# Performance work log

Hardware: AMD Instinct MI355X
Metric: run time of the kernel (lower is better)

Reference implementation:

```python
import jax, jax.numpy as jnp
import numpy as np

GROUPS = 32
HEADS = 8
EPS = 1e-5


def group_norm(x, w, b):
    B, C, H, W = x.shape
    xg = x.reshape(B, GROUPS, C // GROUPS, H, W)
    mu = xg.mean(axis=(2, 3, 4), keepdims=True)
    var = xg.var(axis=(2, 3, 4), keepdims=True)
    xn = ((xg - mu) * jax.lax.rsqrt(var + EPS)).reshape(B, C, H, W)
    return xn * w[None, :, None, None] + b[None, :, None, None]


def conv1x1(x, w, b):
    # w: [out_c, in_c], x: [B, C, H, W]
    return jnp.einsum('oc,bchw->bohw', w, x) + b[None, :, None, None]


def setup_inputs() -> dict:
    key = jax.random.key(0)
    ks = jax.random.split(key, 10)
    B, C, H, W = 8, 512, 32, 32
    s = 1.0 / np.sqrt(C)
    inp = {
        'x': jax.random.normal(ks[0], (B, C, H, W), dtype=jnp.float32),
        'gn_w': jnp.ones((C,), jnp.float32),
        'gn_b': jnp.zeros((C,), jnp.float32),
        'qw': jax.random.uniform(ks[1], (C, C), jnp.float32, -s, s),
        'qb': jax.random.uniform(ks[2], (C,), jnp.float32, -s, s),
        'kw': jax.random.uniform(ks[3], (C, C), jnp.float32, -s, s),
        'kb': jax.random.uniform(ks[4], (C,), jnp.float32, -s, s),
        'vw': jax.random.uniform(ks[5], (C, C), jnp.float32, -s, s),
        'vb': jax.random.uniform(ks[6], (C,), jnp.float32, -s, s),
        'ow': jax.random.uniform(ks[7], (C, C), jnp.float32, -s, s),
        'ob': jax.random.uniform(ks[8], (C,), jnp.float32, -s, s),
    }
    return inp


def reference(x, gn_w, gn_b, qw, qb, kw, kb, vw, vb, ow, ob):
    B, C, H, W = x.shape
    hd = C // HEADS          # head_dim
    N = H * W                # spatial tokens
    scale = float(hd) ** -0.5

    xn = group_norm(x, gn_w, gn_b)
    q = conv1x1(xn, qw, qb).reshape(B, HEADS, hd, N)
    k = conv1x1(xn, kw, kb).reshape(B, HEADS, hd, N)
    v = conv1x1(xn, vw, vb).reshape(B, HEADS, hd, N)

    # scores[b,h,n,m] = scale * <q[:, :, :, n], k[:, :, :, m]>
    scores = jnp.einsum('bhdn,bhdm->bhnm', q * scale, k)
    attn = jax.nn.softmax(scores, axis=-1)
    # out[b,h,d,n] = sum_m attn[b,h,n,m] * v[b,h,d,m]
    out = jnp.einsum('bhnm,bhdm->bhdn', attn, v).reshape(B, C, H, W)
    out = conv1x1(out, ow, ob)
    return out + x
```

## Files before the change

### kernel.cpp

```cpp
#include <hip/hip_runtime.h>
#include <cstdint>


typedef unsigned short u16;
typedef __attribute__((ext_vector_type(8)))  __bf16 bf16x8;
typedef __attribute__((ext_vector_type(4)))  float  f32x4;
typedef __attribute__((ext_vector_type(16))) float  f32x16;

typedef __attribute__((address_space(1))) const unsigned int guint;
typedef __attribute__((address_space(3))) unsigned int       luint;

__device__ __forceinline__ u16 f2bf(float f) {
  union { float f; unsigned u; } a; a.f = f;
  unsigned r = a.u + 0x7fffu + ((a.u >> 16) & 1u);
  return (u16)(r >> 16);
}

__device__ __forceinline__ unsigned pkbf(float a, float b) {
  unsigned short lo = __builtin_bit_cast(unsigned short, (__bf16)a);
  unsigned short hi = __builtin_bit_cast(unsigned short, (__bf16)b);
  return (unsigned)lo | ((unsigned)hi << 16);
}

__device__ __forceinline__ void plswap(unsigned &a, unsigned &b) {
  asm("v_permlane32_swap_b32 %0, %1" : "+v"(a), "+v"(b));
}

__device__ __forceinline__ void gload16(u16* lds_dst, const u16* g_src) {
  __builtin_amdgcn_global_load_lds((guint*)g_src, (luint*)lds_dst, 16, 0, 0);
}

__global__ __launch_bounds__(256) void gn_stats(const float* __restrict__ x,
                                                float* __restrict__ pstat) {
  int id = blockIdx.x;
  int bg = id >> 1, chunk = id & 1;
  int tid = threadIdx.x;
  const float* xg = x + ((size_t)(bg * 16 + chunk * 8)) * 1024;
  float s1 = 0.f, s2 = 0.f;
#pragma unroll
  for (int it = 0; it < 8; ++it) {
    f32x4 v = *(const f32x4*)(xg + it * 1024 + tid * 4);
    s1 += (v[0] + v[1]) + (v[2] + v[3]);
    s2 += (v[0] * v[0] + v[1] * v[1]) + (v[2] * v[2] + v[3] * v[3]);
  }
#pragma unroll
  for (int d = 32; d; d >>= 1) { s1 += __shfl_down(s1, d, 64); s2 += __shfl_down(s2, d, 64); }
  __shared__ float redw[4][2];
  if ((tid & 63) == 0) { redw[tid >> 6][0] = s1; redw[tid >> 6][1] = s2; }
  __syncthreads();
  if (tid == 0) {
    float t1 = redw[0][0] + redw[1][0] + redw[2][0] + redw[3][0];
    float t2 = redw[0][1] + redw[1][1] + redw[2][1] + redw[3][1];
    pstat[(bg * 2 + chunk) * 2 + 0] = t1;
    pstat[(bg * 2 + chunk) * 2 + 1] = t2;
  }
}

__global__ __launch_bounds__(256) void gn_apply(const float* __restrict__ x,
                                                const float* __restrict__ pstat,
                                                const float* __restrict__ gw,
                                                const float* __restrict__ gb,
                                                u16* __restrict__ xnT) {
  __shared__ u16 tr[64 * 130];
  int id = blockIdx.x;
  int cs = id & 3, ntl = (id >> 2) & 15, b = id >> 6;
  int tid = threadIdx.x;
  int tc = tid >> 1, th = tid & 1;
  int c = cs * 128 + tc, g = c >> 4;
  float a1 = pstat[(b * 32 + g) * 4 + 0], a2 = pstat[(b * 32 + g) * 4 + 1];
  float b1 = pstat[(b * 32 + g) * 4 + 2], b2 = pstat[(b * 32 + g) * 4 + 3];
  float s1 = a1 + b1, s2 = a2 + b2;
  float mean = s1 * (1.f / 16384.f);
  float var  = s2 * (1.f / 16384.f) - mean * mean;
  float rinv = rsqrtf(var + 1e-5f);
  float wgt = gw[c] * rinv;
  float bia = gb[c] - mean * wgt;
  const float* src = x + ((size_t)(b * 512 + c)) * 1024 + ntl * 64 + th * 32;
#pragma unroll
  for (int i = 0; i < 8; ++i) {
    f32x4 v = *(const f32x4*)(src + i * 4);
#pragma unroll
    for (int j = 0; j < 4; ++j)
      tr[(th * 32 + i * 4 + j) * 130 + tc] = f2bf(v[j] * wgt + bia);
  }
  __syncthreads();
  int n = tid >> 2, q = tid & 3;
  u16* dst = xnT + (size_t)b * 524288 + (size_t)(ntl * 64 + n) * 512 + cs * 128 + q * 32;
#pragma unroll
  for (int wd = 0; wd < 16; ++wd)
    *(unsigned*)&dst[wd * 2] = *(const unsigned*)&tr[n * 130 + q * 32 + wd * 2];
}

__global__ __launch_bounds__(256) void cvtw_kernel(const float* __restrict__ q,
                                                   const float* __restrict__ k,
                                                   const float* __restrict__ v,
                                                   const float* __restrict__ o,
                                                   u16* __restrict__ dst) {
  int i = blockIdx.x * 256 + threadIdx.x;
  int wsel = i >> 16;
  const float* src = wsel == 0 ? q : wsel == 1 ? k : wsel == 2 ? v : o;
  f32x4 val = *(const f32x4*)(src + (size_t)(i & 65535) * 4);
  u16 r0 = f2bf(val[0]), r1 = f2bf(val[1]), r2 = f2bf(val[2]), r3 = f2bf(val[3]);
  unsigned lo = (unsigned)r0 | ((unsigned)r1 << 16);
  unsigned hi = (unsigned)r2 | ((unsigned)r3 << 16);
  unsigned long long pk = (unsigned long long)lo | ((unsigned long long)hi << 32);
  *(unsigned long long*)(dst + (size_t)i * 4) = pk;
}

__global__ __launch_bounds__(256) void gemm_qkv(
    const u16* __restrict__ xnT, const u16* __restrict__ Wc,
    const float* __restrict__ qb, const float* __restrict__ kb,
    const float* __restrict__ vb,
    u16* __restrict__ Qs, u16* __restrict__ Ks, u16* __restrict__ Vs) {
  __shared__ u16 smem[32768];
  int id = blockIdx.x;
  int xcd = id & 7, slot = id >> 3;
  int g12 = slot / 12, q12 = slot % 12;
  int p = xcd * 8 + g12;
  int b = p & 7, yt = p >> 3;
  int xt = q12 & 3, which = q12 >> 2;

  const u16* Ab = xnT + (size_t)b * 524288 + (size_t)yt * 128 * 512;
  const u16* Bb = Wc + which * 262144 + (size_t)xt * 128 * 512;
  const float* bias = which == 0 ? qb : (which == 1 ? kb : vb);
  float scale = which == 0 ? 0.18033688011112043f : 1.0f;

  int tid = threadIdx.x, w = tid >> 6, lane = tid & 63;
  int wr = w >> 1, wcn = w & 1;
  int srow = lane >> 3, sk8 = (lane & 7) ^ srow;
  f32x4 acc[4][4] = {};

#define QKV_STAGE(buf, k0)                                                     \
  {                                                                            \
    u16* lA_ = smem + (buf) * 8192;                                            \
    u16* lB_ = smem + 16384 + (buf) * 8192;                                    \
    _Pragma("unroll")                                                          \
    for (int c2 = 0; c2 < 4; ++c2) {                                           \
      int ck = w * 4 + c2;                                                     \
      gload16(&lA_[ck * 512], Ab + (size_t)(ck * 8 + srow) * 512 + (k0) + sk8 * 8); \
      gload16(&lB_[ck * 512], Bb + (size_t)(ck * 8 + srow) * 512 + (k0) + sk8 * 8); \
    }                                                                          \
  }

  QKV_STAGE(0, 0);
  __syncthreads();
  for (int t = 0; t < 8; ++t) {
    if (t < 7) QKV_STAGE((t + 1) & 1, (t + 1) * 64);
    const u16* lA = smem + (t & 1) * 8192;
    const u16* lB = smem + 16384 + (t & 1) * 8192;
#pragma unroll
    for (int ks = 0; ks < 2; ++ks) {
      int k8 = ks * 4 + (lane >> 4);
      bf16x8 af[4], bfr[4];
#pragma unroll
      for (int mf = 0; mf < 4; ++mf) {
        int row = wr * 64 + mf * 16 + (lane & 15);
        af[mf] = *(const bf16x8*)&lA[row * 64 + ((k8 ^ (row & 7)) * 8)];
      }
#pragma unroll
      for (int nf = 0; nf < 4; ++nf) {
        int row = wcn * 64 + nf * 16 + (lane & 15);
        bfr[nf] = *(const bf16x8*)&lB[row * 64 + ((k8 ^ (row & 7)) * 8)];
      }
#pragma unroll
      for (int mf = 0; mf < 4; ++mf)
#pragma unroll
        for (int nf = 0; nf < 4; ++nf)
          acc[mf][nf] = __builtin_amdgcn_mfma_f32_16x16x32_bf16(af[mf], bfr[nf], acc[mf][nf], 0, 0, 0);
    }
    __syncthreads();
  }
#undef QKV_STAGE

  if (which < 2) {
    u16* dst = (which == 0 ? Qs : Ks) + (size_t)b * 524288;
#pragma unroll
    for (int mf = 0; mf < 4; ++mf)
#pragma unroll
      for (int nf = 0; nf < 4; ++nf) {
        int cc = xt * 128 + wcn * 64 + nf * 16 + (lane & 15);
        float bv = bias[cc];
#pragma unroll
        for (int j = 0; j < 4; ++j) {
          int rr = yt * 128 + wr * 64 + mf * 16 + (lane >> 4) * 4 + j;
          dst[(size_t)rr * 512 + cc] = f2bf((acc[mf][nf][j] + bv) * scale);
        }
      }
  } else {
    u16* tr = smem;
#pragma unroll
    for (int mf = 0; mf < 4; ++mf)
#pragma unroll
      for (int nf = 0; nf < 4; ++nf) {
        int cc_t = wcn * 64 + nf * 16 + (lane & 15);
        float bv = bias[xt * 128 + cc_t];
#pragma unroll
        for (int j = 0; j < 4; ++j) {
          int rr_t = wr * 64 + mf * 16 + (lane >> 4) * 4 + j;
          tr[cc_t * 136 + rr_t] = f2bf(acc[mf][nf][j] + bv);
        }
      }
    __syncthreads();
    int r = tid >> 1, half = tid & 1;
    size_t base = (size_t)b * 524288 + (size_t)(xt * 128 + r) * 1024 + yt * 128 + half * 64;
#pragma unroll
    for (int i = 0; i < 8; ++i) {
      bf16x8 v = *(const bf16x8*)&tr[r * 136 + half * 64 + i * 8];
      *(bf16x8*)&Vs[base + i * 8] = v;
    }
  }
}

__global__ __launch_bounds__(256) void attn_kernel(const u16* __restrict__ Q,
                                                   const u16* __restrict__ Kt,
                                                   const u16* __restrict__ V,
                                                   u16* __restrict__ AO) {
  __shared__ __align__(16) u16 lK[2][8192];
  __shared__ __align__(16) u16 lV[2][8192];
  int id = blockIdx.x;
  int xcd = id & 7, slot = id >> 3;
  int bh = xcd * 8 + (slot >> 3);
  int nt = slot & 7;
  int b = bh >> 3, h = bh & 7;
  int tid = threadIdx.x, w = tid >> 6, lane = tid & 63;
  int l31 = lane & 31, lh = lane >> 5, r7 = l31 & 7;
  int nb = nt * 128 + w * 32;
  const u16* Qb = Q  + (size_t)b * 524288;
  const u16* Kb = Kt + (size_t)b * 524288 + h * 64;
  const u16* Vb = V  + (size_t)b * 524288 + (size_t)(h * 64) * 1024;

  int srowK = lane >> 3, sblkK = (lane & 7) ^ srowK;
  int srowV = lane >> 4;

  int kblk[4];
#pragma unroll
  for (int kc = 0; kc < 4; ++kc) kblk[kc] = ((kc * 2 + lh) ^ r7) * 8;

  bf16x8 bq[4];
#pragma unroll
  for (int kc = 0; kc < 4; ++kc)
    bq[kc] = *(const bf16x8*)&Qb[(size_t)(nb + l31) * 512 + h * 64 + kc * 16 + lh * 8];

  union { unsigned u[4]; bf16x8 v; } uo;
  uo.u[0] = uo.u[1] = uo.u[2] = uo.u[3] = 0x3F803F80u;
  bf16x8 vones = uo.v;

  f32x16 o0 = {}, o1 = {}, osum = {};

#define ATTN_STAGE(buf, m0)                                                    \
  {                                                                            \
    _Pragma("unroll")                                                          \
    for (int c2 = 0; c2 < 4; ++c2) {                                           \
      int ck = w * 4 + c2;                                                     \
      gload16(&lK[buf][ck * 512],                                              \
              Kb + (size_t)((m0) + ck * 8 + srowK) * 512 + sblkK * 8);         \
      int rv = ck * 4 + srowV;                                                 \
      int bvb = (lane & 15) ^ (rv & 7);                                        \
      gload16(&lV[buf][ck * 512], Vb + (size_t)rv * 1024 + (m0) + bvb * 8);    \
    }                                                                          \
  }

  ATTN_STAGE(0, 0);
  __syncthreads();
  for (int mt = 0; mt < 8; ++mt) {
    int cur = mt & 1;
    if (mt < 7) ATTN_STAGE(cur ^ 1, (mt + 1) * 128);
    const u16* kb = lK[cur];
    const u16* vb = lV[cur];
#pragma unroll
    for (int mb = 0; mb < 4; ++mb) {
      f32x16 s = {};
      int krow = (mb * 32 + l31) * 64;
#pragma unroll
      for (int kc = 0; kc < 4; ++kc) {
        bf16x8 ak = *(const bf16x8*)&kb[krow + kblk[kc]];
        s = __builtin_amdgcn_mfma_f32_32x32x16_bf16(ak, bq[kc], s, 0, 0, 0);
      }
      float p[16];
#pragma unroll
      for (int i = 0; i < 16; ++i) p[i] = exp2f(s[i]);
      unsigned A0 = pkbf(p[0], p[1]),  B0 = pkbf(p[4], p[5]);
      unsigned A1 = pkbf(p[2], p[3]),  B1 = pkbf(p[6], p[7]);
      unsigned A2 = pkbf(p[8], p[9]),  B2 = pkbf(p[12], p[13]);
      unsigned A3 = pkbf(p[10], p[11]), B3 = pkbf(p[14], p[15]);
      plswap(A0, B0); plswap(A1, B1); plswap(A2, B2); plswap(A3, B3);
      union { unsigned u[4]; bf16x8 v; } f0, f1;
      f0.u[0] = A0; f0.u[1] = A1; f0.u[2] = B0; f0.u[3] = B1;
      f1.u[0] = A2; f1.u[1] = A3; f1.u[2] = B2; f1.u[3] = B3;
#pragma unroll
      for (int kc = 0; kc < 2; ++kc) {
        bf16x8 pa = kc ? f1.v : f0.v;
        int vb0 = ((mb * 4 + kc * 2 + lh) ^ r7) * 8;
        bf16x8 v0 = *(const bf16x8*)&vb[(l31) * 128 + vb0];
        bf16x8 v1 = *(const bf16x8*)&vb[(32 + l31) * 128 + vb0];
        o0 = __builtin_amdgcn_mfma_f32_32x32x16_bf16(pa, v0, o0, 0, 0, 0);
        o1 = __builtin_amdgcn_mfma_f32_32x32x16_bf16(pa, v1, o1, 0, 0, 0);
        osum = __builtin_amdgcn_mfma_f32_32x32x16_bf16(pa, vones, osum, 0, 0, 0);
      }
    }
    __syncthreads();
  }
#undef ATTN_STAGE

  size_t base = (size_t)b * 524288;
#pragma unroll
  for (int i = 0; i < 16; ++i) {
    float rl = 1.0f / osum[i];
    int n = nb + (i & 3) + 8 * (i >> 2) + 4 * lh;
    size_t rowb = base + (size_t)n * 512 + h * 64;
    AO[rowb + l31]      = f2bf(o0[i] * rl);
    AO[rowb + 32 + l31] = f2bf(o1[i] * rl);
  }
}

__global__ __launch_bounds__(256) void gemm_proj(
    const u16* __restrict__ Wo, const u16* __restrict__ AO,
    const float* __restrict__ ob, const float* __restrict__ x,
    float* __restrict__ out) {
  __shared__ u16 smem[24576];
  int id = blockIdx.x;
  int xcd = id & 7, slot = id >> 3;
  int g8 = slot >> 3, y = slot & 7;
  int p = xcd * 8 + g8;
  int b = p & 7, xt = p >> 3;

  const u16* Ab = Wo + (size_t)y * 64 * 512;
  const u16* Bb = AO + (size_t)b * 524288 + (size_t)xt * 128 * 512;

  int tid = threadIdx.x, w = tid >> 6, lane = tid & 63;
  int wr = w >> 1, wcn = w & 1;
  int srow = lane >> 3, sk8 = (lane & 7) ^ srow;
  f32x4 acc[2][4] = {};

#define PROJ_STAGE(buf, k0)                                                    \
  {                                                                            \
    u16* lA_ = smem + (buf) * 4096;                                            \
    u16* lB_ = smem + 8192 + (buf) * 8192;                                     \
    _Pragma("unroll")                                                          \
    for (int c2 = 0; c2 < 6; ++c2) {                                           \
      int ck = w * 6 + c2;                                                     \
      if (ck < 8)                                                              \
        gload16(&lA_[ck * 512], Ab + (size_t)(ck * 8 + srow) * 512 + (k0) + sk8 * 8); \
      else                                                                     \
        gload16(&lB_[(ck - 8) * 512], Bb + (size_t)((ck - 8) * 8 + srow) * 512 + (k0) + sk8 * 8); \
    }                                                                          \
  }

  PROJ_STAGE(0, 0);
  __syncthreads();
  for (int t = 0; t < 8; ++t) {
    if (t < 7) PROJ_STAGE((t + 1) & 1, (t + 1) * 64);
    const u16* lA = smem + (t & 1) * 4096;
    const u16* lB = smem + 8192 + (t & 1) * 8192;
#pragma unroll
    for (int ks = 0; ks < 2; ++ks) {
      int k8 = ks * 4 + (lane >> 4);
      bf16x8 af[2], bfr[4];
#pragma unroll
      for (int mf = 0; mf < 2; ++mf) {
        int row = wr * 32 + mf * 16 + (lane & 15);
        af[mf] = *(const bf16x8*)&lA[row * 64 + ((k8 ^ (row & 7)) * 8)];
      }
#pragma unroll
      for (int nf = 0; nf < 4; ++nf) {
        int row = wcn * 64 + nf * 16 + (lane & 15);
        bfr[nf] = *(const bf16x8*)&lB[row * 64 + ((k8 ^ (row & 7)) * 8)];
      }
#pragma unroll
      for (int mf = 0; mf < 2; ++mf)
#pragma unroll
        for (int nf = 0; nf < 4; ++nf)
          acc[mf][nf] = __builtin_amdgcn_mfma_f32_16x16x32_bf16(af[mf], bfr[nf], acc[mf][nf], 0, 0, 0);
    }
    __syncthreads();
  }
#undef PROJ_STAGE

#pragma unroll
  for (int mf = 0; mf < 2; ++mf)
#pragma unroll
    for (int nf = 0; nf < 4; ++nf) {
      int cc = xt * 128 + wcn * 64 + nf * 16 + (lane & 15);
#pragma unroll
      for (int j = 0; j < 4; ++j) {
        int rr = y * 64 + wr * 32 + mf * 16 + (lane >> 4) * 4 + j;
        size_t idx = (size_t)b * 524288 + (size_t)rr * 1024 + cc;
        out[idx] = acc[mf][nf][j] + ob[rr] + x[idx];
      }
    }
}

extern "C" void kernel_launch(void* const* d_in, const int* in_sizes, int n_in,
                              void* d_out, int out_size, void* d_ws, size_t ws_size,
                              hipStream_t stream) {
  const float* x   = (const float*)d_in[0];
  const float* gnw = (const float*)d_in[1];
  const float* gnb = (const float*)d_in[2];
  const float* qw  = (const float*)d_in[3];
  const float* qb  = (const float*)d_in[4];
  const float* kw  = (const float*)d_in[5];
  const float* kb  = (const float*)d_in[6];
  const float* vw  = (const float*)d_in[7];
  const float* vb  = (const float*)d_in[8];
  const float* ow  = (const float*)d_in[9];
  const float* ob  = (const float*)d_in[10];
  float* out = (float*)d_out;

  u16* ws  = (u16*)d_ws;
  u16* xnT = ws;
  u16* Qs  = ws + 4194304;
  u16* Ks  = ws + 8388608;
  u16* Vs  = ws + 12582912;
  u16* Wc  = ws + 16777216;
  float* pstat = (float*)(ws + 17825792);
  u16* AO  = xnT;

  gn_stats<<<512, 256, 0, stream>>>(x, pstat);
  gn_apply<<<512, 256, 0, stream>>>(x, pstat, gnw, gnb, xnT);
  cvtw_kernel<<<1024, 256, 0, stream>>>(qw, kw, vw, ow, Wc);
  gemm_qkv<<<768, 256, 0, stream>>>(xnT, Wc, qb, kb, vb, Qs, Ks, Vs);
  attn_kernel<<<512, 256, 0, stream>>>(Qs, Ks, Vs, AO);
  gemm_proj<<<512, 256, 0, stream>>>(Wc + 786432, AO, ob, x, out);
}
```

Measured before the change: 166.7 us.

## Replace ones-MFMA row sum with lane sums and shrink attention KV tiles

Drops the third MFMA per PV step, which multiplied P by a vector of ones to get softmax denominators. Each lane now sums its exp values in scalar registers, the two half-waves are combined with a shuffle, and the result is redistributed through a small per-wave LDS buffer. The KV tile shrinks from 128 to 64 keys, halving LDS use, with a padded, swizzled layout shared by K and V. s_setprio hints are placed around the MFMA blocks. This cuts matrix-core work and LDS footprint, at the cost of more loop iterations and barriers plus extra VALU adds.

```diff
diff --git a/kernel.cpp b/kernel.cpp
--- a/kernel.cpp
+++ b/kernel.cpp
@@ -215,8 +215,9 @@
                                                    const u16* __restrict__ Kt,
                                                    const u16* __restrict__ V,
                                                    u16* __restrict__ AO) {
-  __shared__ __align__(16) u16 lK[2][8192];
-  __shared__ __align__(16) u16 lV[2][8192];
+  __shared__ __align__(16) u16 lK[2][4160];
+  __shared__ __align__(16) u16 lV[2][4160];
+  __shared__ __align__(16) float lsum[4][32];
   int id = blockIdx.x;
   int xcd = id & 7, slot = id >> 3;
   int bh = xcd * 8 + (slot >> 3);
@@ -229,87 +230,97 @@
   const u16* Kb = Kt + (size_t)b * 524288 + h * 64;
   const u16* Vb = V  + (size_t)b * 524288 + (size_t)(h * 64) * 1024;
 
-  int srowK = lane >> 3, sblkK = (lane & 7) ^ srowK;
-  int srowV = lane >> 4;
-
-  int kblk[4];
-#pragma unroll
-  for (int kc = 0; kc < 4; ++kc) kblk[kc] = ((kc * 2 + lh) ^ r7) * 8;
-
+  int lrow = lane >> 3, lblk = (lane & 7) ^ lrow;
+
+  int kbase = (l31 >> 3) * 520 + r7 * 64;
   bf16x8 bq[4];
 #pragma unroll
   for (int kc = 0; kc < 4; ++kc)
     bq[kc] = *(const bf16x8*)&Qb[(size_t)(nb + l31) * 512 + h * 64 + kc * 16 + lh * 8];
 
-  union { unsigned u[4]; bf16x8 v; } uo;
-  uo.u[0] = uo.u[1] = uo.u[2] = uo.u[3] = 0x3F803F80u;
-  bf16x8 vones = uo.v;
-
-  f32x16 o0 = {}, o1 = {}, osum = {};
+  f32x16 o0 = {}, o1 = {};
+  float lpart = 0.f;
 
 #define ATTN_STAGE(buf, m0)                                                    \
   {                                                                            \
     _Pragma("unroll")                                                          \
-    for (int c2 = 0; c2 < 4; ++c2) {                                           \
-      int ck = w * 4 + c2;                                                     \
-      gload16(&lK[buf][ck * 512],                                              \
-              Kb + (size_t)((m0) + ck * 8 + srowK) * 512 + sblkK * 8);         \
-      int rv = ck * 4 + srowV;                                                 \
-      int bvb = (lane & 15) ^ (rv & 7);                                        \
-      gload16(&lV[buf][ck * 512], Vb + (size_t)rv * 1024 + (m0) + bvb * 8);    \
+    for (int c2 = 0; c2 < 2; ++c2) {                                           \
+      int ck = w * 2 + c2;                                                     \
+      gload16(&lK[buf][ck * 520],                                              \
+              Kb + (size_t)((m0) + ck * 8 + lrow) * 512 + lblk * 8);           \
+      gload16(&lV[buf][ck * 520],                                              \
+              Vb + (size_t)(ck * 8 + lrow) * 1024 + (m0) + lblk * 8);          \
     }                                                                          \
   }
 
   ATTN_STAGE(0, 0);
   __syncthreads();
-  for (int mt = 0; mt < 8; ++mt) {
+  for (int mt = 0; mt < 16; ++mt) {
     int cur = mt & 1;
-    if (mt < 7) ATTN_STAGE(cur ^ 1, (mt + 1) * 128);
+    if (mt < 15) ATTN_STAGE(cur ^ 1, (mt + 1) * 64);
     const u16* kb = lK[cur];
     const u16* vb = lV[cur];
 #pragma unroll
-    for (int mb = 0; mb < 4; ++mb) {
+    for (int mb = 0; mb < 2; ++mb) {
       f32x16 s = {};
-      int krow = (mb * 32 + l31) * 64;
+      int kroff = mb * 2080 + kbase;
+      __builtin_amdgcn_s_setprio(1);
 #pragma unroll
       for (int kc = 0; kc < 4; ++kc) {
-        bf16x8 ak = *(const bf16x8*)&kb[krow + kblk[kc]];
+        bf16x8 ak = *(const bf16x8*)&kb[kroff + (((kc * 2 + lh) ^ r7) * 8)];
         s = __builtin_amdgcn_mfma_f32_32x32x16_bf16(ak, bq[kc], s, 0, 0, 0);
       }
+      __builtin_amdgcn_s_setprio(0);
       float p[16];
 #pragma unroll
       for (int i = 0; i < 16; ++i) p[i] = exp2f(s[i]);
-      unsigned A0 = pkbf(p[0], p[1]),  B0 = pkbf(p[4], p[5]);
-      unsigned A1 = pkbf(p[2], p[3]),  B1 = pkbf(p[6], p[7]);
-      unsigned A2 = pkbf(p[8], p[9]),  B2 = pkbf(p[12], p[13]);
+      lpart += ((p[0] + p[1]) + (p[2] + p[3])) + ((p[4] + p[5]) + (p[6] + p[7]))
+             + ((p[8] + p[9]) + (p[10] + p[11])) + ((p[12] + p[13]) + (p[14] + p[15]));
+      unsigned A0 = pkbf(p[0], p[1]),   B0 = pkbf(p[4], p[5]);
+      unsigned A1 = pkbf(p[2], p[3]),   B1 = pkbf(p[6], p[7]);
+      unsigned A2 = pkbf(p[8], p[9]),   B2 = pkbf(p[12], p[13]);
       unsigned A3 = pkbf(p[10], p[11]), B3 = pkbf(p[14], p[15]);
       plswap(A0, B0); plswap(A1, B1); plswap(A2, B2); plswap(A3, B3);
       union { unsigned u[4]; bf16x8 v; } f0, f1;
       f0.u[0] = A0; f0.u[1] = A1; f0.u[2] = B0; f0.u[3] = B1;
       f1.u[0] = A2; f1.u[1] = A3; f1.u[2] = B2; f1.u[3] = B3;
+      __builtin_amdgcn_s_setprio(1);
 #pragma unroll
       for (int kc = 0; kc < 2; ++kc) {
         bf16x8 pa = kc ? f1.v : f0.v;
-        int vb0 = ((mb * 4 + kc * 2 + lh) ^ r7) * 8;
-        bf16x8 v0 = *(const bf16x8*)&vb[(l31) * 128 + vb0];
-        bf16x8 v1 = *(const bf16x8*)&vb[(32 + l31) * 128 + vb0];
+        int vblk = ((mb * 4 + kc * 2 + lh) ^ r7) * 8;
+        bf16x8 v0 = *(const bf16x8*)&vb[kbase + vblk];
+        bf16x8 v1 = *(const bf16x8*)&vb[2080 + kbase + vblk];
         o0 = __builtin_amdgcn_mfma_f32_32x32x16_bf16(pa, v0, o0, 0, 0, 0);
         o1 = __builtin_amdgcn_mfma_f32_32x32x16_bf16(pa, v1, o1, 0, 0, 0);
-        osum = __builtin_amdgcn_mfma_f32_32x32x16_bf16(pa, vones, osum, 0, 0, 0);
-      }
+      }
+      __builtin_amdgcn_s_setprio(0);
     }
     __syncthreads();
   }
 #undef ATTN_STAGE
 
+  lpart += __shfl_xor(lpart, 32, 64);
+  if (lh == 0) lsum[w][l31] = lpart;
+  f32x4 s0 = *(const f32x4*)&lsum[w][4 * lh];
+  f32x4 s1 = *(const f32x4*)&lsum[w][8 + 4 * lh];
+  f32x4 s2 = *(const f32x4*)&lsum[w][16 + 4 * lh];
+  f32x4 s3 = *(const f32x4*)&lsum[w][24 + 4 * lh];
+  float rl[16];
+#pragma unroll
+  for (int j = 0; j < 4; ++j) {
+    rl[j]      = 1.0f / s0[j];
+    rl[4 + j]  = 1.0f / s1[j];
+    rl[8 + j]  = 1.0f / s2[j];
+    rl[12 + j] = 1.0f / s3[j];
+  }
   size_t base = (size_t)b * 524288;
 #pragma unroll
   for (int i = 0; i < 16; ++i) {
-    float rl = 1.0f / osum[i];
     int n = nb + (i & 3) + 8 * (i >> 2) + 4 * lh;
     size_t rowb = base + (size_t)n * 512 + h * 64;
-    AO[rowb + l31]      = f2bf(o0[i] * rl);
-    AO[rowb + 32 + l31] = f2bf(o1[i] * rl);
+    AO[rowb + l31]      = f2bf(o0[i] * rl[i]);
+    AO[rowb + 32 + l31] = f2bf(o1[i] * rl[i]);
   }
 }
 
```

Result: no change. 167.0 us (+0.1%).
